# Kernel optimization log

Hardware: AMD Instinct MI355X
Metric: run time of the kernel (lower is better)

Reference implementation:

```python
import jax, jax.numpy as jnp
import numpy as np

B, N, K = 4, 50000, 128   # batch, surface points, deformation nodes
GD = 128                  # SDF grid resolution (D=H=W)


def setup_inputs() -> dict:
    key = jax.random.key(0)
    ks = jax.random.split(key, 7)
    constants = jax.random.normal(ks[0], (B, K), dtype=jnp.float32)
    scales = 0.05 + 0.25 * jax.random.uniform(ks[1], (B, K), dtype=jnp.float32)
    # proper-ish rotations via QR of random matrices
    M = jax.random.normal(ks[2], (B, K, 3, 3), dtype=jnp.float32)
    rotations, _ = jnp.linalg.qr(M)
    centers = jax.random.uniform(ks[3], (B, K, 3), dtype=jnp.float32, minval=-0.5, maxval=0.5)
    surface_samples = jax.random.uniform(ks[4], (B, N, 6), dtype=jnp.float32, minval=-0.5, maxval=0.5)
    grid = jax.random.normal(ks[5], (B, GD, GD, GD), dtype=jnp.float32)
    # world2grid maps world [-0.5,0.5] -> grid index [0, GD-1]
    w2g = np.zeros((B, 4, 4), dtype=np.float32)
    w2g[:, 0, 0] = w2g[:, 1, 1] = w2g[:, 2, 2] = float(GD - 1)
    w2g[:, :3, 3] = float(GD - 1) / 2.0
    w2g[:, 3, 3] = 1.0
    world2grid = jnp.asarray(w2g)
    return {"constants": constants, "scales": scales, "rotations": rotations,
            "centers": centers, "surface_samples": surface_samples,
            "grid": grid, "world2grid": world2grid}


def _trilinear_border(vol, xyz):
    """torch grid_sample (5D, bilinear, align_corners=True, border) for one batch.
    vol: (D,H,W); xyz: (N,3) normalized coords in [-1,1], order (x,y,z)."""
    D, H, W = vol.shape
    x = jnp.clip((xyz[:, 0] + 1.0) * 0.5 * (W - 1), 0.0, W - 1)
    y = jnp.clip((xyz[:, 1] + 1.0) * 0.5 * (H - 1), 0.0, H - 1)
    z = jnp.clip((xyz[:, 2] + 1.0) * 0.5 * (D - 1), 0.0, D - 1)
    x0 = jnp.floor(x); y0 = jnp.floor(y); z0 = jnp.floor(z)
    fx = x - x0; fy = y - y0; fz = z - z0
    x0i = x0.astype(jnp.int32); x1i = jnp.minimum(x0i + 1, W - 1)
    y0i = y0.astype(jnp.int32); y1i = jnp.minimum(y0i + 1, H - 1)
    z0i = z0.astype(jnp.int32); z1i = jnp.minimum(z0i + 1, D - 1)
    c000 = vol[z0i, y0i, x0i]; c001 = vol[z0i, y0i, x1i]
    c010 = vol[z0i, y1i, x0i]; c011 = vol[z0i, y1i, x1i]
    c100 = vol[z1i, y0i, x0i]; c101 = vol[z1i, y0i, x1i]
    c110 = vol[z1i, y1i, x0i]; c111 = vol[z1i, y1i, x1i]
    c00 = c000 * (1 - fx) + c001 * fx
    c01 = c010 * (1 - fx) + c011 * fx
    c10 = c100 * (1 - fx) + c101 * fx
    c11 = c110 * (1 - fx) + c111 * fx
    c0 = c00 * (1 - fy) + c01 * fy
    c1 = c10 * (1 - fy) + c11 * fy
    return c0 * (1 - fz) + c1 * fz


def reference(constants, scales, rotations, centers, surface_samples, grid, world2grid):
    pts = surface_samples[..., :3]                       # (B,N,3)
    diff = pts[:, :, None, :] - centers[:, None, :, :]   # (B,N,K,3)  == p - t_source
    d2 = jnp.sum(diff * diff, axis=-1)                   # (B,N,K)
    # sample_rbf_weights with use_constants=True
    w = jnp.exp(-d2 / (2.0 * scales * scales)[:, None, :]) * (constants * constants)[:, None, :]
    w = w / jnp.sum(w, axis=-1, keepdims=True)           # normalize over nodes

    # target = roll batch by -1 (source_idx+1 mod B)
    R_t = jnp.roll(rotations, -1, axis=0)
    R_rel = jnp.einsum('bkij,bklj->bkil', R_t, rotations)       # R_target @ R_source^T
    c_t = jnp.roll(centers, -1, axis=0)
    transformed = jnp.einsum('bkij,bnkj->bnki', R_rel, diff) + c_t[:, None, :, :]
    blended = jnp.einsum('bnk,bnki->bni', w, transformed)        # (B,N,3)

    w2g_t = jnp.roll(world2grid, -1, axis=0)
    A = w2g_t[:, :3, :3]
    t = w2g_t[:, :3, 3]
    gcs = jnp.einsum('bij,bnj->bni', A, blended) + t[:, None, :]  # grid coords (x,y,z)

    D, H, W = grid.shape[1], grid.shape[2], grid.shape[3]
    denom = jnp.array([W - 1, H - 1, D - 1], dtype=gcs.dtype)
    gcs = 2.0 * (gcs / denom) - 1.0                               # normalize to [-1,1]

    grid_t = jnp.roll(grid, -1, axis=0)
    sdf = jax.vmap(_trilinear_border)(grid_t, gcs)                # (B,N)
    return jnp.sum(jnp.mean(sdf * sdf, axis=1))
```

## Files before the change

### kernel.cpp

```cpp
#include <hip/hip_runtime.h>

#define K_   128
#define GD_  128
#define PSTR 20

static __device__ __forceinline__ float fast_exp2(float x) {
#if __has_builtin(__builtin_amdgcn_exp2f)
    return __builtin_amdgcn_exp2f(x);
#else
    return exp2f(x);
#endif
}

__global__ void surf_param_kernel(
    const float* __restrict__ constants,
    const float* __restrict__ scales,
    const float* __restrict__ rotations,
    const float* __restrict__ centers,
    const float* __restrict__ w2g,
    float* __restrict__ params,
    float* __restrict__ out,
    int B)
{
    int idx = blockIdx.x * blockDim.x + threadIdx.x;
    if (idx == 0) out[0] = 0.0f;
    if (idx >= B * K_) return;
    int b = idx / K_, k = idx - b * K_;
    int bn = (b + 1 == B) ? 0 : (b + 1);
    const float L2E = 1.4426950408889634f;

    const float* R  = rotations + (size_t)(b  * K_ + k) * 9;
    const float* Rt = rotations + (size_t)(bn * K_ + k) * 9;
    float m[9];
#pragma unroll
    for (int i = 0; i < 3; ++i)
#pragma unroll
        for (int l = 0; l < 3; ++l)
            m[i * 3 + l] = Rt[i * 3 + 0] * R[l * 3 + 0]
                         + Rt[i * 3 + 1] * R[l * 3 + 1]
                         + Rt[i * 3 + 2] * R[l * 3 + 2];

    const float* Aw = w2g + (size_t)bn * 16;
    float G[9], A[9] = {Aw[0], Aw[1], Aw[2], Aw[4], Aw[5], Aw[6], Aw[8], Aw[9], Aw[10]};
    float T[3] = {Aw[3], Aw[7], Aw[11]};
#pragma unroll
    for (int i = 0; i < 3; ++i)
#pragma unroll
        for (int l = 0; l < 3; ++l)
            G[i * 3 + l] = A[i * 3 + 0] * m[0 * 3 + l]
                         + A[i * 3 + 1] * m[1 * 3 + l]
                         + A[i * 3 + 2] * m[2 * 3 + l];

    const float* c  = centers + (size_t)(b  * K_ + k) * 3;
    const float* ct = centers + (size_t)(bn * K_ + k) * 3;
    float c0 = c[0], c1 = c[1], c2 = c[2];
    float vw0 = ct[0] - (m[0] * c0 + m[1] * c1 + m[2] * c2);
    float vw1 = ct[1] - (m[3] * c0 + m[4] * c1 + m[5] * c2);
    float vw2 = ct[2] - (m[6] * c0 + m[7] * c1 + m[8] * c2);
    float v0 = A[0] * vw0 + A[1] * vw1 + A[2] * vw2 + T[0];
    float v1 = A[3] * vw0 + A[4] * vw1 + A[5] * vw2 + T[1];
    float v2 = A[6] * vw0 + A[7] * vw1 + A[8] * vw2 + T[2];

    float sig = scales[b * K_ + k];
    float s   = 1.0f / (2.0f * sig * sig);
    float con = constants[b * K_ + k];
    float s2n = -s * L2E;
    float r   = log2f(con * con) + s2n * (c0 * c0 + c1 * c1 + c2 * c2);

    float* o = params + (size_t)idx * PSTR;
    o[0] = G[0]; o[1] = G[1]; o[2] = G[2]; o[3] = G[3];
    o[4] = G[4]; o[5] = G[5]; o[6] = G[6]; o[7] = G[7];
    o[8] = G[8]; o[9] = v0;  o[10] = v1;  o[11] = v2;
    o[12] = -2.0f * s2n * c0;
    o[13] = -2.0f * s2n * c1;
    o[14] = -2.0f * s2n * c2;
    o[15] = r;
    o[16] = s2n;
    o[17] = 0.f; o[18] = 0.f; o[19] = 0.f;
}

__global__ __launch_bounds__(256) void surf_loss_kernel(
    const float* __restrict__ sp,
    const float* __restrict__ grid,
    const float* __restrict__ params,
    float* __restrict__ out,
    int N, int B, int bpb)
{
    __shared__ float lds[K_ * PSTR];
    const int tid = threadIdx.x;
    const int blk = blockIdx.x;
    const int b   = blk / bpb;
    const int n   = (blk - b * bpb) * 256 + tid;
    const bool valid = (n < N);
    const int bn  = (b + 1 == B) ? 0 : (b + 1);

    {
        const float4* Pv = (const float4*)(params + (size_t)b * K_ * PSTR);
        float4* Lv = (float4*)lds;
#pragma unroll
        for (int t = tid; t < K_ * PSTR / 4; t += 256)
            Lv[t] = Pv[t];
    }

    const float* qp = sp + ((size_t)b * N + (valid ? n : 0)) * 6;
    float px = qp[0], py = qp[1], pz = qp[2];
    float pq = px * px + py * py + pz * pz;
    float ax = 0.f, ay = 0.f, az = 0.f, aw = 0.f;

    __syncthreads();

#pragma unroll 2
    for (int k = 0; k < K_; ++k) {
        const float4* f = (const float4*)(lds + k * PSTR);
        const float4 f0 = f[0];
        const float4 f1 = f[1];
        const float4 f2 = f[2];
        const float4 f3 = f[3];
        const float  s2 = lds[k * PSTR + 16];

        float e = f3.w + f3.x * px + f3.y * py + f3.z * pz + s2 * pq;
        float w = fast_exp2(e);
        float tx = f2.y + f0.x * px + f0.y * py + f0.z * pz;
        float ty = f2.z + f0.w * px + f1.x * py + f1.y * pz;
        float tz = f2.w + f1.z * px + f1.w * py + f2.x * pz;
        ax += w * tx;
        ay += w * ty;
        az += w * tz;
        aw += w;
    }

    float accum = 0.0f;
    if (valid) {
        float inv = 1.0f / aw;
        float x = fminf(fmaxf(ax * inv, 0.0f), (float)(GD_ - 1));
        float y = fminf(fmaxf(ay * inv, 0.0f), (float)(GD_ - 1));
        float z = fminf(fmaxf(az * inv, 0.0f), (float)(GD_ - 1));
        float x0f = floorf(x), y0f = floorf(y), z0f = floorf(z);
        float fx = x - x0f, fy = y - y0f, fz = z - z0f;
        int x0 = (int)x0f, y0 = (int)y0f, z0 = (int)z0f;
        int x1 = x0 + 1 > GD_ - 1 ? GD_ - 1 : x0 + 1;
        int y1 = y0 + 1 > GD_ - 1 ? GD_ - 1 : y0 + 1;
        int z1 = z0 + 1 > GD_ - 1 ? GD_ - 1 : z0 + 1;
        const float* gb = grid + (size_t)bn * GD_ * GD_ * GD_;
        int zy00 = (z0 * GD_ + y0) * GD_;
        int zy01 = (z0 * GD_ + y1) * GD_;
        int zy10 = (z1 * GD_ + y0) * GD_;
        int zy11 = (z1 * GD_ + y1) * GD_;
        float c000 = gb[zy00 + x0], c001 = gb[zy00 + x1];
        float c010 = gb[zy01 + x0], c011 = gb[zy01 + x1];
        float c100 = gb[zy10 + x0], c101 = gb[zy10 + x1];
        float c110 = gb[zy11 + x0], c111 = gb[zy11 + x1];
        float ofx = 1.0f - fx, ofy = 1.0f - fy, ofz = 1.0f - fz;
        float c00 = c000 * ofx + c001 * fx;
        float c01 = c010 * ofx + c011 * fx;
        float c10 = c100 * ofx + c101 * fx;
        float c11 = c110 * ofx + c111 * fx;
        float c0 = c00 * ofy + c01 * fy;
        float c1 = c10 * ofy + c11 * fy;
        float sdf = c0 * ofz + c1 * fz;
        accum = sdf * sdf;
    }

    __shared__ float red[4];
#pragma unroll
    for (int off = 32; off > 0; off >>= 1)
        accum += __shfl_down(accum, off, 64);
    int wave = tid >> 6;
    if ((tid & 63) == 0) red[wave] = accum;
    __syncthreads();
    if (tid == 0)
        atomicAdd(out, (red[0] + red[1] + red[2] + red[3]) * (1.0f / (float)N));
}

extern "C" void kernel_launch(void* const* d_in, const int* in_sizes, int n_in,
                              void* d_out, int out_size, void* d_ws, size_t ws_size,
                              hipStream_t stream) {
    const float* constants = (const float*)d_in[0];
    const float* scales    = (const float*)d_in[1];
    const float* rotations = (const float*)d_in[2];
    const float* centers   = (const float*)d_in[3];
    const float* sp        = (const float*)d_in[4];
    const float* grid      = (const float*)d_in[5];
    const float* w2g       = (const float*)d_in[6];
    float* out = (float*)d_out;
    float* params = (float*)d_ws;

    const int B = in_sizes[6] / 16;
    const int N = in_sizes[4] / (6 * B);

    int np = B * K_;
    hipLaunchKernelGGL(surf_param_kernel, dim3((np + 255) / 256), dim3(256), 0, stream,
                       constants, scales, rotations, centers, w2g, params, out, B);

    const int bpb = (N + 255) / 256;
    hipLaunchKernelGGL(surf_loss_kernel, dim3(B * bpb), dim3(256), 0, stream,
                       sp, grid, params, out, N, B, bpb);
}
```

Before: 119.9 us.

## Read node params via scalar constant loads and process two points per thread

The per-node parameters are now read straight from global memory through the constant address space, so the compiler can issue wave-uniform scalar loads in place of the LDS staging and block barrier. Each thread now handles two surface points, so every parameter fetch is reused across both points. The risks are more registers per thread and half as many blocks, which means less parallelism for the 200k points.

```diff
diff --git a/kernel.cpp b/kernel.cpp
--- a/kernel.cpp
+++ b/kernel.cpp
@@ -1,8 +1,13 @@
 #include <hip/hip_runtime.h>
+#include <stdint.h>
 
 #define K_   128
 #define GD_  128
 #define PSTR 20
+
+typedef float vf4 __attribute__((ext_vector_type(4)));
+typedef const __attribute__((address_space(4))) float  cfloat;
+typedef const __attribute__((address_space(4))) vf4    cvf4;
 
 static __device__ __forceinline__ float fast_exp2(float x) {
 #if __has_builtin(__builtin_amdgcn_exp2f)
@@ -79,6 +84,7 @@
     o[17] = 0.f; o[18] = 0.f; o[19] = 0.f;
 }
 
+#define PPT 2
 __global__ __launch_bounds__(256) void surf_loss_kernel(
     const float* __restrict__ sp,
     const float* __restrict__ grid,
@@ -86,62 +92,65 @@
     float* __restrict__ out,
     int N, int B, int bpb)
 {
-    __shared__ float lds[K_ * PSTR];
     const int tid = threadIdx.x;
     const int blk = blockIdx.x;
     const int b   = blk / bpb;
-    const int n   = (blk - b * bpb) * 256 + tid;
-    const bool valid = (n < N);
+    const int n0  = (blk - b * bpb) * (256 * PPT) + tid;
     const int bn  = (b + 1 == B) ? 0 : (b + 1);
 
-    {
-        const float4* Pv = (const float4*)(params + (size_t)b * K_ * PSTR);
-        float4* Lv = (float4*)lds;
-#pragma unroll
-        for (int t = tid; t < K_ * PSTR / 4; t += 256)
-            Lv[t] = Pv[t];
+    cfloat* Pc = (cfloat*)(uintptr_t)(params + (size_t)b * K_ * PSTR);
+
+    float px[PPT], py[PPT], pz[PPT], pq[PPT];
+    float ax[PPT], ay[PPT], az[PPT], aw[PPT];
+    bool  valid[PPT];
+    const float* spb = sp + (size_t)b * N * 6;
+#pragma unroll
+    for (int j = 0; j < PPT; ++j) {
+        int n = n0 + 256 * j;
+        valid[j] = (n < N);
+        const float* q = spb + (size_t)(valid[j] ? n : 0) * 6;
+        px[j] = q[0]; py[j] = q[1]; pz[j] = q[2];
+        pq[j] = px[j] * px[j] + py[j] * py[j] + pz[j] * pz[j];
+        ax[j] = 0.f; ay[j] = 0.f; az[j] = 0.f; aw[j] = 0.f;
     }
-
-    const float* qp = sp + ((size_t)b * N + (valid ? n : 0)) * 6;
-    float px = qp[0], py = qp[1], pz = qp[2];
-    float pq = px * px + py * py + pz * pz;
-    float ax = 0.f, ay = 0.f, az = 0.f, aw = 0.f;
-
-    __syncthreads();
 
 #pragma unroll 2
     for (int k = 0; k < K_; ++k) {
-        const float4* f = (const float4*)(lds + k * PSTR);
-        const float4 f0 = f[0];
-        const float4 f1 = f[1];
-        const float4 f2 = f[2];
-        const float4 f3 = f[3];
-        const float  s2 = lds[k * PSTR + 16];
-
-        float e = f3.w + f3.x * px + f3.y * py + f3.z * pz + s2 * pq;
-        float w = fast_exp2(e);
-        float tx = f2.y + f0.x * px + f0.y * py + f0.z * pz;
-        float ty = f2.z + f0.w * px + f1.x * py + f1.y * pz;
-        float tz = f2.w + f1.z * px + f1.w * py + f2.x * pz;
-        ax += w * tx;
-        ay += w * ty;
-        az += w * tz;
-        aw += w;
+        cfloat* o = Pc + k * PSTR;
+        vf4 f0 = ((cvf4*)o)[0];
+        vf4 f1 = ((cvf4*)o)[1];
+        vf4 f2 = ((cvf4*)o)[2];
+        vf4 f3 = ((cvf4*)o)[3];
+        float s2 = o[16];
+#pragma unroll
+        for (int j = 0; j < PPT; ++j) {
+            float e = f3.w + f3.x * px[j] + f3.y * py[j] + f3.z * pz[j] + s2 * pq[j];
+            float w = fast_exp2(e);
+            float tx = f2.y + f0.x * px[j] + f0.y * py[j] + f0.z * pz[j];
+            float ty = f2.z + f0.w * px[j] + f1.x * py[j] + f1.y * pz[j];
+            float tz = f2.w + f1.z * px[j] + f1.w * py[j] + f2.x * pz[j];
+            ax[j] += w * tx;
+            ay[j] += w * ty;
+            az[j] += w * tz;
+            aw[j] += w;
+        }
     }
 
+    const float* gb = grid + (size_t)bn * GD_ * GD_ * GD_;
     float accum = 0.0f;
-    if (valid) {
-        float inv = 1.0f / aw;
-        float x = fminf(fmaxf(ax * inv, 0.0f), (float)(GD_ - 1));
-        float y = fminf(fmaxf(ay * inv, 0.0f), (float)(GD_ - 1));
-        float z = fminf(fmaxf(az * inv, 0.0f), (float)(GD_ - 1));
+#pragma unroll
+    for (int j = 0; j < PPT; ++j) {
+        if (!valid[j]) continue;
+        float inv = 1.0f / aw[j];
+        float x = fminf(fmaxf(ax[j] * inv, 0.0f), (float)(GD_ - 1));
+        float y = fminf(fmaxf(ay[j] * inv, 0.0f), (float)(GD_ - 1));
+        float z = fminf(fmaxf(az[j] * inv, 0.0f), (float)(GD_ - 1));
         float x0f = floorf(x), y0f = floorf(y), z0f = floorf(z);
         float fx = x - x0f, fy = y - y0f, fz = z - z0f;
         int x0 = (int)x0f, y0 = (int)y0f, z0 = (int)z0f;
         int x1 = x0 + 1 > GD_ - 1 ? GD_ - 1 : x0 + 1;
         int y1 = y0 + 1 > GD_ - 1 ? GD_ - 1 : y0 + 1;
         int z1 = z0 + 1 > GD_ - 1 ? GD_ - 1 : z0 + 1;
-        const float* gb = grid + (size_t)bn * GD_ * GD_ * GD_;
         int zy00 = (z0 * GD_ + y0) * GD_;
         int zy01 = (z0 * GD_ + y1) * GD_;
         int zy10 = (z1 * GD_ + y0) * GD_;
@@ -158,7 +167,7 @@
         float c0 = c00 * ofy + c01 * fy;
         float c1 = c10 * ofy + c11 * fy;
         float sdf = c0 * ofz + c1 * fz;
-        accum = sdf * sdf;
+        accum += sdf * sdf;
     }
 
     __shared__ float red[4];
@@ -192,7 +201,8 @@
     hipLaunchKernelGGL(surf_param_kernel, dim3((np + 255) / 256), dim3(256), 0, stream,
                        constants, scales, rotations, centers, w2g, params, out, B);
 
-    const int bpb = (N + 255) / 256;
+    const int ppb = 256 * PPT;
+    const int bpb = (N + ppb - 1) / ppb;
     hipLaunchKernelGGL(surf_loss_kernel, dim3(B * bpb), dim3(256), 0, stream,
                        sp, grid, params, out, N, B, bpb);
 }
```

After: 124.1 us. +3.5%, slower.

## Split node loop across waves with 4 points per thread and LDS reduction

Applied to the files above, without the earlier changes.

Each wave now handles 32 of the 128 deformation nodes for all 256 points of the block, with each thread holding 4 points in registers. Partial weighted sums are written to LDS and reduced across waves before the trilinear SDF lookup. This reuses each LDS parameter fetch across 4 points, cutting LDS read traffic per FLOP and adding independent exp/FMA chains for ILP. The costs are more registers (16 accumulators plus 16 point values), an extra LDS buffer and barrier, and a different summation order for the weights.

```diff
diff --git a/kernel.cpp b/kernel.cpp
--- a/kernel.cpp
+++ b/kernel.cpp
@@ -1,8 +1,10 @@
 #include <hip/hip_runtime.h>
+#include <stdint.h>
 
 #define K_   128
 #define GD_  128
 #define PSTR 20
+#define KPW  32
 
 static __device__ __forceinline__ float fast_exp2(float x) {
 #if __has_builtin(__builtin_amdgcn_exp2f)
@@ -86,87 +88,113 @@
     float* __restrict__ out,
     int N, int B, int bpb)
 {
-    __shared__ float lds[K_ * PSTR];
-    const int tid = threadIdx.x;
-    const int blk = blockIdx.x;
-    const int b   = blk / bpb;
-    const int n   = (blk - b * bpb) * 256 + tid;
-    const bool valid = (n < N);
-    const int bn  = (b + 1 == B) ? 0 : (b + 1);
+    __shared__ float  lds_par[K_ * PSTR];
+    __shared__ float4 lds_part[4 * 4 * 64];
+    __shared__ float  red[4];
+
+    const int tid  = threadIdx.x;
+    const int lane = tid & 63;
+    const int wave = tid >> 6;
+    const int blk  = blockIdx.x;
+    const int b    = blk / bpb;
+    const int base = (blk - b * bpb) * 256;
+    const int bn   = (b + 1 == B) ? 0 : (b + 1);
 
     {
         const float4* Pv = (const float4*)(params + (size_t)b * K_ * PSTR);
-        float4* Lv = (float4*)lds;
-#pragma unroll
+        float4* Lv = (float4*)lds_par;
         for (int t = tid; t < K_ * PSTR / 4; t += 256)
             Lv[t] = Pv[t];
     }
 
-    const float* qp = sp + ((size_t)b * N + (valid ? n : 0)) * 6;
-    float px = qp[0], py = qp[1], pz = qp[2];
-    float pq = px * px + py * py + pz * pz;
-    float ax = 0.f, ay = 0.f, az = 0.f, aw = 0.f;
+    float px[4], py[4], pz[4], pq[4];
+    float ax[4], ay[4], az[4], aw[4];
+    const float* spb = sp + (size_t)b * N * 6;
+#pragma unroll
+    for (int j = 0; j < 4; ++j) {
+        int n = base + j * 64 + lane;
+        int nn = (n < N) ? n : 0;
+        const float* q = spb + (size_t)nn * 6;
+        px[j] = q[0]; py[j] = q[1]; pz[j] = q[2];
+        pq[j] = px[j] * px[j] + py[j] * py[j] + pz[j] * pz[j];
+        ax[j] = 0.f; ay[j] = 0.f; az[j] = 0.f; aw[j] = 0.f;
+    }
 
     __syncthreads();
 
+    const int k0 = wave * KPW;
 #pragma unroll 2
-    for (int k = 0; k < K_; ++k) {
-        const float4* f = (const float4*)(lds + k * PSTR);
+    for (int kk = 0; kk < KPW; ++kk) {
+        const float4* f = (const float4*)(lds_par + (k0 + kk) * PSTR);
         const float4 f0 = f[0];
         const float4 f1 = f[1];
         const float4 f2 = f[2];
         const float4 f3 = f[3];
-        const float  s2 = lds[k * PSTR + 16];
-
-        float e = f3.w + f3.x * px + f3.y * py + f3.z * pz + s2 * pq;
-        float w = fast_exp2(e);
-        float tx = f2.y + f0.x * px + f0.y * py + f0.z * pz;
-        float ty = f2.z + f0.w * px + f1.x * py + f1.y * pz;
-        float tz = f2.w + f1.z * px + f1.w * py + f2.x * pz;
-        ax += w * tx;
-        ay += w * ty;
-        az += w * tz;
-        aw += w;
-    }
+        const float  s2 = lds_par[(k0 + kk) * PSTR + 16];
+#pragma unroll
+        for (int j = 0; j < 4; ++j) {
+            float e = f3.w + f3.x * px[j] + f3.y * py[j] + f3.z * pz[j] + s2 * pq[j];
+            float w = fast_exp2(e);
+            float tx = f2.y + f0.x * px[j] + f0.y * py[j] + f0.z * pz[j];
+            float ty = f2.z + f0.w * px[j] + f1.x * py[j] + f1.y * pz[j];
+            float tz = f2.w + f1.z * px[j] + f1.w * py[j] + f2.x * pz[j];
+            ax[j] += w * tx;
+            ay[j] += w * ty;
+            az[j] += w * tz;
+            aw[j] += w;
+        }
+    }
+
+#pragma unroll
+    for (int j = 0; j < 4; ++j)
+        lds_part[((wave * 4 + j) << 6) + lane] = make_float4(ax[j], ay[j], az[j], aw[j]);
+    __syncthreads();
 
     float accum = 0.0f;
-    if (valid) {
-        float inv = 1.0f / aw;
-        float x = fminf(fmaxf(ax * inv, 0.0f), (float)(GD_ - 1));
-        float y = fminf(fmaxf(ay * inv, 0.0f), (float)(GD_ - 1));
-        float z = fminf(fmaxf(az * inv, 0.0f), (float)(GD_ - 1));
-        float x0f = floorf(x), y0f = floorf(y), z0f = floorf(z);
-        float fx = x - x0f, fy = y - y0f, fz = z - z0f;
-        int x0 = (int)x0f, y0 = (int)y0f, z0 = (int)z0f;
-        int x1 = x0 + 1 > GD_ - 1 ? GD_ - 1 : x0 + 1;
-        int y1 = y0 + 1 > GD_ - 1 ? GD_ - 1 : y0 + 1;
-        int z1 = z0 + 1 > GD_ - 1 ? GD_ - 1 : z0 + 1;
-        const float* gb = grid + (size_t)bn * GD_ * GD_ * GD_;
-        int zy00 = (z0 * GD_ + y0) * GD_;
-        int zy01 = (z0 * GD_ + y1) * GD_;
-        int zy10 = (z1 * GD_ + y0) * GD_;
-        int zy11 = (z1 * GD_ + y1) * GD_;
-        float c000 = gb[zy00 + x0], c001 = gb[zy00 + x1];
-        float c010 = gb[zy01 + x0], c011 = gb[zy01 + x1];
-        float c100 = gb[zy10 + x0], c101 = gb[zy10 + x1];
-        float c110 = gb[zy11 + x0], c111 = gb[zy11 + x1];
-        float ofx = 1.0f - fx, ofy = 1.0f - fy, ofz = 1.0f - fz;
-        float c00 = c000 * ofx + c001 * fx;
-        float c01 = c010 * ofx + c011 * fx;
-        float c10 = c100 * ofx + c101 * fx;
-        float c11 = c110 * ofx + c111 * fx;
-        float c0 = c00 * ofy + c01 * fy;
-        float c1 = c10 * ofy + c11 * fy;
-        float sdf = c0 * ofz + c1 * fz;
-        accum = sdf * sdf;
-    }
-
-    __shared__ float red[4];
+    {
+        int n = base + wave * 64 + lane;
+        if (n < N) {
+            float sx = 0.f, sy = 0.f, sz = 0.f, sw = 0.f;
+#pragma unroll
+            for (int w = 0; w < 4; ++w) {
+                float4 t = lds_part[((w * 4 + wave) << 6) + lane];
+                sx += t.x; sy += t.y; sz += t.z; sw += t.w;
+            }
+            float inv = 1.0f / sw;
+            float x = fminf(fmaxf(sx * inv, 0.0f), (float)(GD_ - 1));
+            float y = fminf(fmaxf(sy * inv, 0.0f), (float)(GD_ - 1));
+            float z = fminf(fmaxf(sz * inv, 0.0f), (float)(GD_ - 1));
+            float x0f = floorf(x), y0f = floorf(y), z0f = floorf(z);
+            float fx = x - x0f, fy = y - y0f, fz = z - z0f;
+            int x0 = (int)x0f, y0 = (int)y0f, z0 = (int)z0f;
+            int x1 = x0 + 1 > GD_ - 1 ? GD_ - 1 : x0 + 1;
+            int y1 = y0 + 1 > GD_ - 1 ? GD_ - 1 : y0 + 1;
+            int z1 = z0 + 1 > GD_ - 1 ? GD_ - 1 : z0 + 1;
+            const float* gb = grid + (size_t)bn * GD_ * GD_ * GD_;
+            int zy00 = (z0 * GD_ + y0) * GD_;
+            int zy01 = (z0 * GD_ + y1) * GD_;
+            int zy10 = (z1 * GD_ + y0) * GD_;
+            int zy11 = (z1 * GD_ + y1) * GD_;
+            float c000 = gb[zy00 + x0], c001 = gb[zy00 + x1];
+            float c010 = gb[zy01 + x0], c011 = gb[zy01 + x1];
+            float c100 = gb[zy10 + x0], c101 = gb[zy10 + x1];
+            float c110 = gb[zy11 + x0], c111 = gb[zy11 + x1];
+            float ofx = 1.0f - fx, ofy = 1.0f - fy, ofz = 1.0f - fz;
+            float c00 = c000 * ofx + c001 * fx;
+            float c01 = c010 * ofx + c011 * fx;
+            float c10 = c100 * ofx + c101 * fx;
+            float c11 = c110 * ofx + c111 * fx;
+            float c0 = c00 * ofy + c01 * fy;
+            float c1 = c10 * ofy + c11 * fy;
+            float sdf = c0 * ofz + c1 * fz;
+            accum = sdf * sdf;
+        }
+    }
+
 #pragma unroll
     for (int off = 32; off > 0; off >>= 1)
         accum += __shfl_down(accum, off, 64);
-    int wave = tid >> 6;
-    if ((tid & 63) == 0) red[wave] = accum;
+    if (lane == 0) red[wave] = accum;
     __syncthreads();
     if (tid == 0)
         atomicAdd(out, (red[0] + red[1] + red[2] + red[3]) * (1.0f / (float)N));
```

After: 113.1 us. -5.7%, faster.

## Split node loop across waves and read params via scalar constant loads

Applied to the files above, without the earlier changes.

Each block now handles 64 points, and its four waves each process a quarter of the 128 deformation nodes. Parameters are read through constant-address-space pointers so the loads can become wave-uniform scalar loads instead of LDS reads. Partial sums are combined in shared memory, and wave 0 does the trilinear sample and issues one atomic per wave. The aim is to raise parallelism and drop LDS bandwidth, at the cost of four times as many blocks and atomics and three idle waves during the gather.

```diff
diff --git a/kernel.cpp b/kernel.cpp
--- a/kernel.cpp
+++ b/kernel.cpp
@@ -1,8 +1,14 @@
 #include <hip/hip_runtime.h>
+#include <stdint.h>
 
 #define K_   128
 #define GD_  128
 #define PSTR 20
+#define KPW  32
+
+typedef float vf4 __attribute__((ext_vector_type(4)));
+typedef const __attribute__((address_space(4))) float  cfloat;
+typedef const __attribute__((address_space(4))) vf4    cvf4;
 
 static __device__ __forceinline__ float fast_exp2(float x) {
 #if __has_builtin(__builtin_amdgcn_exp2f)
@@ -79,44 +85,39 @@
     o[17] = 0.f; o[18] = 0.f; o[19] = 0.f;
 }
 
-__global__ __launch_bounds__(256) void surf_loss_kernel(
+__global__ __launch_bounds__(256, 8) void surf_loss_kernel(
     const float* __restrict__ sp,
     const float* __restrict__ grid,
     const float* __restrict__ params,
     float* __restrict__ out,
     int N, int B, int bpb)
 {
-    __shared__ float lds[K_ * PSTR];
-    const int tid = threadIdx.x;
-    const int blk = blockIdx.x;
-    const int b   = blk / bpb;
-    const int n   = (blk - b * bpb) * 256 + tid;
-    const bool valid = (n < N);
-    const int bn  = (b + 1 == B) ? 0 : (b + 1);
-
-    {
-        const float4* Pv = (const float4*)(params + (size_t)b * K_ * PSTR);
-        float4* Lv = (float4*)lds;
-#pragma unroll
-        for (int t = tid; t < K_ * PSTR / 4; t += 256)
-            Lv[t] = Pv[t];
-    }
-
-    const float* qp = sp + ((size_t)b * N + (valid ? n : 0)) * 6;
-    float px = qp[0], py = qp[1], pz = qp[2];
+    __shared__ vf4 lds_part[4 * 64];
+
+    const int tid  = threadIdx.x;
+    const int lane = tid & 63;
+    const int wave = tid >> 6;
+    const int blk  = blockIdx.x;
+    const int b    = blk / bpb;
+    const int n    = (blk - b * bpb) * 64 + lane;
+    const int bn   = (b + 1 == B) ? 0 : (b + 1);
+
+    const float* q = sp + ((size_t)b * N + (size_t)((n < N) ? n : 0)) * 6;
+    float px = q[0], py = q[1], pz = q[2];
     float pq = px * px + py * py + pz * pz;
     float ax = 0.f, ay = 0.f, az = 0.f, aw = 0.f;
 
-    __syncthreads();
-
-#pragma unroll 2
-    for (int k = 0; k < K_; ++k) {
-        const float4* f = (const float4*)(lds + k * PSTR);
-        const float4 f0 = f[0];
-        const float4 f1 = f[1];
-        const float4 f2 = f[2];
-        const float4 f3 = f[3];
-        const float  s2 = lds[k * PSTR + 16];
+    cfloat* Pc = (cfloat*)(uintptr_t)(params
+               + ((size_t)b * K_ + (size_t)wave * KPW) * PSTR);
+
+#pragma unroll 4
+    for (int kk = 0; kk < KPW; ++kk) {
+        cfloat* o = Pc + kk * PSTR;
+        vf4 f0 = ((cvf4*)o)[0];
+        vf4 f1 = ((cvf4*)o)[1];
+        vf4 f2 = ((cvf4*)o)[2];
+        vf4 f3 = ((cvf4*)o)[3];
+        float s2 = o[16];
 
         float e = f3.w + f3.x * px + f3.y * py + f3.z * pz + s2 * pq;
         float w = fast_exp2(e);
@@ -129,12 +130,24 @@
         aw += w;
     }
 
+    vf4 part = {ax, ay, az, aw};
+    lds_part[(wave << 6) + lane] = part;
+    __syncthreads();
+    if (wave != 0) return;
+
+    float sx = 0.f, sy = 0.f, sz = 0.f, sw = 0.f;
+#pragma unroll
+    for (int w = 0; w < 4; ++w) {
+        vf4 t = lds_part[(w << 6) + lane];
+        sx += t.x; sy += t.y; sz += t.z; sw += t.w;
+    }
+
     float accum = 0.0f;
-    if (valid) {
-        float inv = 1.0f / aw;
-        float x = fminf(fmaxf(ax * inv, 0.0f), (float)(GD_ - 1));
-        float y = fminf(fmaxf(ay * inv, 0.0f), (float)(GD_ - 1));
-        float z = fminf(fmaxf(az * inv, 0.0f), (float)(GD_ - 1));
+    if (n < N) {
+        float inv = 1.0f / sw;
+        float x = fminf(fmaxf(sx * inv, 0.0f), (float)(GD_ - 1));
+        float y = fminf(fmaxf(sy * inv, 0.0f), (float)(GD_ - 1));
+        float z = fminf(fmaxf(sz * inv, 0.0f), (float)(GD_ - 1));
         float x0f = floorf(x), y0f = floorf(y), z0f = floorf(z);
         float fx = x - x0f, fy = y - y0f, fz = z - z0f;
         int x0 = (int)x0f, y0 = (int)y0f, z0 = (int)z0f;
@@ -161,15 +174,11 @@
         accum = sdf * sdf;
     }
 
-    __shared__ float red[4];
 #pragma unroll
     for (int off = 32; off > 0; off >>= 1)
         accum += __shfl_down(accum, off, 64);
-    int wave = tid >> 6;
-    if ((tid & 63) == 0) red[wave] = accum;
-    __syncthreads();
-    if (tid == 0)
-        atomicAdd(out, (red[0] + red[1] + red[2] + red[3]) * (1.0f / (float)N));
+    if (lane == 0)
+        atomicAdd(out, accum * (1.0f / (float)N));
 }
 
 extern "C" void kernel_launch(void* const* d_in, const int* in_sizes, int n_in,
@@ -192,7 +201,7 @@
     hipLaunchKernelGGL(surf_param_kernel, dim3((np + 255) / 256), dim3(256), 0, stream,
                        constants, scales, rotations, centers, w2g, params, out, B);
 
-    const int bpb = (N + 255) / 256;
+    const int bpb = (N + 63) / 64;
     hipLaunchKernelGGL(surf_loss_kernel, dim3(B * bpb), dim3(256), 0, stream,
                        sp, grid, params, out, N, B, bpb);
 }
```

Result: slower. 154.6 us (+29.0%).
